# Kernel optimization log

Hardware: AMD Instinct MI355X
Metric: run time of the kernel (lower is better)

The kernel has to match this reference:

```python
import jax, jax.numpy as jnp
import numpy as np

IN_F, OUT_F, GS = 4096, 16384, 128


def setup_inputs() -> dict:
    key = jax.random.key(0)
    k1, k2, k3 = jax.random.split(key, 3)
    x = jax.random.normal(k1, (2, 1024, IN_F), dtype=jnp.float32)
    # ternary codes in {-1, 0, 1}, stored as int8 in the original module
    ternary = jax.random.randint(k2, (OUT_F, IN_F), -1, 2, dtype=jnp.int32)
    n_groups = OUT_F * IN_F // GS
    # per-group scales: positive, like beta = mean(|w|) per group
    scales = jax.random.uniform(k3, (n_groups,), dtype=jnp.float32, minval=0.01, maxval=0.1)
    return {"x": x, "ternary": ternary, "scales": scales}


def reference(x, ternary, scales):
    # Dequantize: each contiguous group of GS flattened weight entries shares one scale.
    w = (ternary.astype(jnp.float32).reshape(-1, GS) * scales[:, None]).reshape(OUT_F, IN_F)
    # F.linear(x, w) == x @ w.T
    return jnp.einsum('bsi,oi->bso', x, w)
```

## Files before the change

kernel.cpp:

```cpp
#include <hip/hip_runtime.h>
#include <hip/hip_bf16.h>
#include <stdint.h>

#define M_ROWS 2048
#define IN_F   4096
#define OUT_F  16384

#define BM 128
#define BN 128
#define BK 64

typedef __attribute__((ext_vector_type(8))) short short8;
typedef __attribute__((ext_vector_type(4))) float floatx4;

__device__ __forceinline__ unsigned short f32_to_bf16_rne(float f) {
    union { float f; uint32_t u; } v; v.f = f;
    uint32_t u = v.u;
    return (unsigned short)((u + 0x7FFFu + ((u >> 16) & 1u)) >> 16);
}

__global__ __launch_bounds__(256) void convert_x_kernel(
        const float* __restrict__ x, unsigned short* __restrict__ xb) {
    int t = blockIdx.x * 256 + threadIdx.x;
    const float4* p = (const float4*)(x + (size_t)t * 8);
    float4 a = p[0];
    float4 b = p[1];
    short8 o;
    o[0] = (short)f32_to_bf16_rne(a.x);
    o[1] = (short)f32_to_bf16_rne(a.y);
    o[2] = (short)f32_to_bf16_rne(a.z);
    o[3] = (short)f32_to_bf16_rne(a.w);
    o[4] = (short)f32_to_bf16_rne(b.x);
    o[5] = (short)f32_to_bf16_rne(b.y);
    o[6] = (short)f32_to_bf16_rne(b.z);
    o[7] = (short)f32_to_bf16_rne(b.w);
    *(short8*)(xb + (size_t)t * 8) = o;
}

__global__ __launch_bounds__(256) void dequant_w_kernel(
        const int* __restrict__ tern, const float* __restrict__ scales,
        unsigned short* __restrict__ wb) {
    int g = blockIdx.x * 256 + threadIdx.x;
    float s = scales[g >> 4];
    const int4* p = (const int4*)(tern + (size_t)g * 8);
    int4 a = p[0];
    int4 b = p[1];
    short8 o;
    o[0] = (short)f32_to_bf16_rne((float)a.x * s);
    o[1] = (short)f32_to_bf16_rne((float)a.y * s);
    o[2] = (short)f32_to_bf16_rne((float)a.z * s);
    o[3] = (short)f32_to_bf16_rne((float)a.w * s);
    o[4] = (short)f32_to_bf16_rne((float)b.x * s);
    o[5] = (short)f32_to_bf16_rne((float)b.y * s);
    o[6] = (short)f32_to_bf16_rne((float)b.z * s);
    o[7] = (short)f32_to_bf16_rne((float)b.w * s);
    *(short8*)(wb + (size_t)g * 8) = o;
}

__global__ __launch_bounds__(256, 3) void gemm_bt_kernel(
        const unsigned short* __restrict__ A,
        const unsigned short* __restrict__ B,
        float* __restrict__ C) {
    __shared__ unsigned short As[BM * BK];
    __shared__ unsigned short Bs[BN * BK];

    const int tid  = threadIdx.x;
    const int lane = tid & 63;
    const int quad = lane >> 4;
    const int frow = lane & 15;
    const int r7   = frow & 7;
    const int w    = tid >> 6;
    const int wm   = (w & 1) * 64;
    const int wn   = (w >> 1) * 64;

    const int bm = blockIdx.x * BM;
    const int bn = blockIdx.y * BN;

    floatx4 acc[4][4] = {};

    int a_off[2][4], b_off[2][4];
#pragma unroll
    for (int ks = 0; ks < 2; ++ks) {
        const int j = ks * 4 + quad;
        const int sw = (j ^ r7) * 8;
#pragma unroll
        for (int t2 = 0; t2 < 4; ++t2) {
            a_off[ks][t2] = (wm + t2 * 16 + frow) * BK + sw;
            b_off[ks][t2] = (wn + t2 * 16 + frow) * BK + sw;
        }
    }

    for (int kt = 0; kt < IN_F; kt += BK) {
        __syncthreads();
#pragma unroll
        for (int i = 0; i < 4; ++i) {
            const int c    = 256 * i + tid;
            const int crow = c >> 3;
            const int jg   = (c & 7) ^ (crow & 7);
            const int ub   = (256 * i + (tid & 192)) * 8;
            const unsigned short* ga =
                A + (size_t)(bm + crow) * IN_F + kt + jg * 8;
            const unsigned short* gb =
                B + (size_t)(bn + crow) * IN_F + kt + jg * 8;
            __builtin_amdgcn_global_load_lds(
                (const __attribute__((address_space(1))) void*)ga,
                (__attribute__((address_space(3))) void*)(As + ub), 16, 0, 0);
            __builtin_amdgcn_global_load_lds(
                (const __attribute__((address_space(1))) void*)gb,
                (__attribute__((address_space(3))) void*)(Bs + ub), 16, 0, 0);
        }
        __syncthreads();
#pragma unroll
        for (int ks = 0; ks < 2; ++ks) {
            short8 af[4], bf[4];
#pragma unroll
            for (int t2 = 0; t2 < 4; ++t2) {
                af[t2] = *(const short8*)(As + a_off[ks][t2]);
                bf[t2] = *(const short8*)(Bs + b_off[ks][t2]);
            }
#pragma unroll
            for (int mt = 0; mt < 4; ++mt)
#pragma unroll
                for (int nt = 0; nt < 4; ++nt)
                    acc[mt][nt] = __builtin_amdgcn_mfma_f32_16x16x32_bf16(
                        af[mt], bf[nt], acc[mt][nt], 0, 0, 0);
        }
    }

    const int row0 = bm + wm + quad * 4;
    const int col0 = bn + wn + frow;
#pragma unroll
    for (int mt = 0; mt < 4; ++mt) {
#pragma unroll
        for (int nt = 0; nt < 4; ++nt) {
            float* cp = C + (size_t)(row0 + mt * 16) * OUT_F + (col0 + nt * 16);
#pragma unroll
            for (int r = 0; r < 4; ++r)
                cp[(size_t)r * OUT_F] = acc[mt][nt][r];
        }
    }
}

extern "C" void kernel_launch(void* const* d_in, const int* in_sizes, int n_in,
                              void* d_out, int out_size, void* d_ws, size_t ws_size,
                              hipStream_t stream) {
    const float* x     = (const float*)d_in[0];
    const int*   tern  = (const int*)d_in[1];
    const float* scal  = (const float*)d_in[2];
    float*       out   = (float*)d_out;

    unsigned short* xb = (unsigned short*)d_ws;
    unsigned short* wb = xb + (size_t)M_ROWS * IN_F;

    convert_x_kernel<<<(M_ROWS * IN_F / 8) / 256, 256, 0, stream>>>(x, xb);
    dequant_w_kernel<<<((size_t)OUT_F * IN_F / 8) / 256, 256, 0, stream>>>(tern, scal, wb);
    gemm_bt_kernel<<<dim3(M_ROWS / BM, OUT_F / BN), 256, 0, stream>>>(xb, wb, out);
}
```

Baseline: 678.1 us.

## Fuse ternary weight dequantization into the GEMM B-tile load

Removes the standalone dequant kernel and its bf16 weight buffer, instead loading int32 ternary codes and scales directly in the GEMM, converting them to bf16 in registers and storing into swizzled shared memory. This avoids writing and rereading a full bf16 weight matrix. In exchange each B tile is fetched as int32 (twice the bytes) by every M-block, and uses synchronous register loads instead of direct-to-LDS async loads, adding latency and global traffic inside the main loop.

```diff
diff --git a/kernel.cpp b/kernel.cpp
--- a/kernel.cpp
+++ b/kernel.cpp
@@ -37,29 +37,17 @@
     *(short8*)(xb + (size_t)t * 8) = o;
 }
 
-__global__ __launch_bounds__(256) void dequant_w_kernel(
-        const int* __restrict__ tern, const float* __restrict__ scales,
-        unsigned short* __restrict__ wb) {
-    int g = blockIdx.x * 256 + threadIdx.x;
-    float s = scales[g >> 4];
-    const int4* p = (const int4*)(tern + (size_t)g * 8);
-    int4 a = p[0];
-    int4 b = p[1];
-    short8 o;
-    o[0] = (short)f32_to_bf16_rne((float)a.x * s);
-    o[1] = (short)f32_to_bf16_rne((float)a.y * s);
-    o[2] = (short)f32_to_bf16_rne((float)a.z * s);
-    o[3] = (short)f32_to_bf16_rne((float)a.w * s);
-    o[4] = (short)f32_to_bf16_rne((float)b.x * s);
-    o[5] = (short)f32_to_bf16_rne((float)b.y * s);
-    o[6] = (short)f32_to_bf16_rne((float)b.z * s);
-    o[7] = (short)f32_to_bf16_rne((float)b.w * s);
-    *(short8*)(wb + (size_t)g * 8) = o;
+__device__ __forceinline__ unsigned int pack2(int t0, int t1, float s) {
+    float w0 = (float)t0 * s;
+    float w1 = (float)t1 * s;
+    return __builtin_amdgcn_perm(__float_as_uint(w1), __float_as_uint(w0),
+                                 0x07060302u);
 }
 
-__global__ __launch_bounds__(256, 3) void gemm_bt_kernel(
+__global__ __launch_bounds__(256, 3) void gemm_fused_kernel(
         const unsigned short* __restrict__ A,
-        const unsigned short* __restrict__ B,
+        const int* __restrict__ T,
+        const float* __restrict__ S,
         float* __restrict__ C) {
     __shared__ unsigned short As[BM * BK];
     __shared__ unsigned short Bs[BN * BK];
@@ -75,6 +63,9 @@
 
     const int bm = blockIdx.x * BM;
     const int bn = blockIdx.y * BN;
+
+    const int r0   = tid >> 3;
+    const int jcol = (tid & 7) ^ (r0 & 7);
 
     floatx4 acc[4][4] = {};
 
@@ -92,6 +83,18 @@
 
     for (int kt = 0; kt < IN_F; kt += BK) {
         __syncthreads();
+
+        int4 q0[4], q1[4];
+        float sc[4];
+#pragma unroll
+        for (int i = 0; i < 4; ++i) {
+            const int row = r0 + 32 * i;
+            const int* gp = T + (size_t)(bn + row) * IN_F + kt + jcol * 8;
+            q0[i] = *(const int4*)gp;
+            q1[i] = *(const int4*)(gp + 4);
+            sc[i] = S[(size_t)(bn + row) * 32 + (kt >> 7)];
+        }
+
 #pragma unroll
         for (int i = 0; i < 4; ++i) {
             const int c    = 256 * i + tid;
@@ -100,16 +103,24 @@
             const int ub   = (256 * i + (tid & 192)) * 8;
             const unsigned short* ga =
                 A + (size_t)(bm + crow) * IN_F + kt + jg * 8;
-            const unsigned short* gb =
-                B + (size_t)(bn + crow) * IN_F + kt + jg * 8;
             __builtin_amdgcn_global_load_lds(
                 (const __attribute__((address_space(1))) void*)ga,
                 (__attribute__((address_space(3))) void*)(As + ub), 16, 0, 0);
-            __builtin_amdgcn_global_load_lds(
-                (const __attribute__((address_space(1))) void*)gb,
-                (__attribute__((address_space(3))) void*)(Bs + ub), 16, 0, 0);
         }
+
+#pragma unroll
+        for (int i = 0; i < 4; ++i) {
+            const float s = __uint_as_float(__float_as_uint(sc[i]) + 0x8000u);
+            int4 o;
+            o.x = (int)pack2(q0[i].x, q0[i].y, s);
+            o.y = (int)pack2(q0[i].z, q0[i].w, s);
+            o.z = (int)pack2(q1[i].x, q1[i].y, s);
+            o.w = (int)pack2(q1[i].z, q1[i].w, s);
+            *(int4*)(Bs + (size_t)(256 * i + tid) * 8) = o;
+        }
+
         __syncthreads();
+
 #pragma unroll
         for (int ks = 0; ks < 2; ++ks) {
             short8 af[4], bf[4];
@@ -144,15 +155,14 @@
 extern "C" void kernel_launch(void* const* d_in, const int* in_sizes, int n_in,
                               void* d_out, int out_size, void* d_ws, size_t ws_size,
                               hipStream_t stream) {
-    const float* x     = (const float*)d_in[0];
-    const int*   tern  = (const int*)d_in[1];
-    const float* scal  = (const float*)d_in[2];
-    float*       out   = (float*)d_out;
+    const float* x    = (const float*)d_in[0];
+    const int*   tern = (const int*)d_in[1];
+    const float* scal = (const float*)d_in[2];
+    float*       out  = (float*)d_out;
 
     unsigned short* xb = (unsigned short*)d_ws;
-    unsigned short* wb = xb + (size_t)M_ROWS * IN_F;
 
     convert_x_kernel<<<(M_ROWS * IN_F / 8) / 256, 256, 0, stream>>>(x, xb);
-    dequant_w_kernel<<<((size_t)OUT_F * IN_F / 8) / 256, 256, 0, stream>>>(tern, scal, wb);
-    gemm_bt_kernel<<<dim3(M_ROWS / BM, OUT_F / BN), 256, 0, stream>>>(xb, wb, out);
+    gemm_fused_kernel<<<dim3(M_ROWS / BM, OUT_F / BN), 256, 0, stream>>>(
+        xb, tern, scal, out);
 }
```

Result: slower. 788.7 us (+16.3%).
